# Kernel optimization log

Measured on AMD Instinct MI355X. Metric: run time of the kernel, lower is better.

## Reference

```python
import jax, jax.numpy as jnp
import numpy as np

B, S, CTX, DIM, NH, FFN, NE, TOPK = 2, 2048, 512, 1536, 12, 6144, 4, 2
HD = DIM // NH
EPS = 1e-6


def lin(x, w, b):
    return jnp.einsum('...d,od->...o', x, w) + b


def rmsnorm(x, w):
    xf = x.astype(jnp.float32)
    n = xf * jax.lax.rsqrt(jnp.mean(xf * xf, axis=-1, keepdims=True) + EPS)
    return n.astype(x.dtype) * w


def layernorm(x, w=None, b=None):
    m = jnp.mean(x, -1, keepdims=True)
    v = jnp.mean((x - m) ** 2, -1, keepdims=True)
    y = (x - m) * jax.lax.rsqrt(v + EPS)
    return y if w is None else y * w + b


def rope(x, cos, sin):
    # x: [B,S,DIM]; complex rotation on consecutive pairs per head
    b, s, _ = x.shape
    xr = x.reshape(b, s, NH, HD // 2, 2)
    xa, xb = xr[..., 0], xr[..., 1]
    c = cos[None, :, None, :]
    sn = sin[None, :, None, :]
    return jnp.stack([xa * c - xb * sn, xa * sn + xb * c], -1).reshape(b, s, DIM)


def sdpa(q, k, v):
    # scaled dot-product attention, q:[B,Sq,DIM], k/v:[B,Sk,DIM]
    b, sq, D = q.shape
    sk = k.shape[1]
    qh = q.reshape(b, sq, NH, HD).transpose(0, 2, 1, 3)
    kh = k.reshape(b, sk, NH, HD).transpose(0, 2, 1, 3)
    vh = v.reshape(b, sk, NH, HD).transpose(0, 2, 1, 3)
    scores = jnp.einsum('bnqd,bnkd->bnqk', qh, kh) * np.float32(1.0 / np.sqrt(HD))
    o = jnp.einsum('bnqk,bnkd->bnqd', jax.nn.softmax(scores, -1), vh)
    return o.transpose(0, 2, 1, 3).reshape(b, sq, D)


def _forward(x, context, t_mod, freqs_cos, freqs_sin, expert_weights,
             sa_q_w, sa_q_b, sa_k_w, sa_k_b, sa_v_w, sa_v_b, sa_o_w, sa_o_b, sa_nq_w, sa_nk_w,
             ca_q_w, ca_q_b, ca_k_w, ca_k_b, ca_v_w, ca_v_b, ca_o_w, ca_o_b, ca_nq_w, ca_nk_w,
             norm3_w, norm3_b, ffn_w1, ffn_b1, ffn_w2, ffn_b2, modulation, moe_w, moe_b,
             top_k_indices):
    mod = modulation + t_mod  # [B,6,DIM]
    shift_msa, scale_msa, gate_msa, shift_mlp, scale_mlp, gate_mlp = jnp.split(mod, 6, axis=1)
    # self-attention with AdaLN modulation + RoPE
    h = layernorm(x) * (1 + scale_msa) + shift_msa
    q = rope(rmsnorm(lin(h, sa_q_w, sa_q_b), sa_nq_w), freqs_cos, freqs_sin)
    k = rope(rmsnorm(lin(h, sa_k_w, sa_k_b), sa_nk_w), freqs_cos, freqs_sin)
    v = lin(h, sa_v_w, sa_v_b)
    x = x + gate_msa * lin(sdpa(q, k, v), sa_o_w, sa_o_b)
    # cross-attention (norm3 has affine params)
    h3 = layernorm(x, norm3_w, norm3_b)
    cq = rmsnorm(lin(h3, ca_q_w, ca_q_b), ca_nq_w)
    ck = rmsnorm(lin(context, ca_k_w, ca_k_b), ca_nk_w)
    cv = lin(context, ca_v_w, ca_v_b)
    x = x + lin(sdpa(cq, ck, cv), ca_o_w, ca_o_b)
    # FFN + MoE branch on the modulated input
    h2 = layernorm(x) * (1 + scale_mlp) + shift_mlp
    ff = lin(jax.nn.gelu(lin(h2, ffn_w1, ffn_b1), approximate=True), ffn_w2, ffn_b2)
    # MoE: compute ALL experts densely (as original), then gather-combine top-k
    eo = jnp.einsum('bsd,eod->bseo', h2, moe_w) + moe_b[None, None]  # [B,S,E,DIM]
    sel = jnp.take_along_axis(eo, top_k_indices[..., None], axis=2)  # [B,S,K,DIM]
    moe_out = jnp.sum(expert_weights[..., None] * sel, axis=2)
    x = x + gate_mlp * (ff + moe_out)
    return x


def setup_inputs() -> dict:
    key = jax.random.key(0)
    ks = iter(jax.random.split(key, 64))
    def rn(shape, scale=0.02):
        return jax.random.normal(next(ks), shape, dtype=jnp.float32) * scale
    pos = jnp.arange(S, dtype=jnp.float32)
    inv = 1.0 / (10000.0 ** (jnp.arange(0, HD, 2, dtype=jnp.float32) / HD))
    ang = pos[:, None] * inv[None, :]  # [S, HD//2]
    ew = jax.random.uniform(next(ks), (B, S, TOPK), dtype=jnp.float32) + 0.1
    ew = ew / jnp.sum(ew, -1, keepdims=True)
    inp = {
        'x': rn((B, S, DIM), 1.0),
        'context': rn((B, CTX, DIM), 1.0),
        't_mod': rn((B, 6, DIM), 1.0),
        'freqs_cos': jnp.cos(ang),
        'freqs_sin': jnp.sin(ang),
        'expert_weights': ew,
        'top_k_indices': jax.random.randint(next(ks), (B, S, TOPK), 0, NE, dtype=jnp.int32),
        'sa_q_w': rn((DIM, DIM)), 'sa_q_b': jnp.zeros((DIM,), jnp.float32),
        'sa_k_w': rn((DIM, DIM)), 'sa_k_b': jnp.zeros((DIM,), jnp.float32),
        'sa_v_w': rn((DIM, DIM)), 'sa_v_b': jnp.zeros((DIM,), jnp.float32),
        'sa_o_w': rn((DIM, DIM)), 'sa_o_b': jnp.zeros((DIM,), jnp.float32),
        'sa_nq_w': jnp.ones((DIM,), jnp.float32), 'sa_nk_w': jnp.ones((DIM,), jnp.float32),
        'ca_q_w': rn((DIM, DIM)), 'ca_q_b': jnp.zeros((DIM,), jnp.float32),
        'ca_k_w': rn((DIM, DIM)), 'ca_k_b': jnp.zeros((DIM,), jnp.float32),
        'ca_v_w': rn((DIM, DIM)), 'ca_v_b': jnp.zeros((DIM,), jnp.float32),
        'ca_o_w': rn((DIM, DIM)), 'ca_o_b': jnp.zeros((DIM,), jnp.float32),
        'ca_nq_w': jnp.ones((DIM,), jnp.float32), 'ca_nk_w': jnp.ones((DIM,), jnp.float32),
        'norm3_w': jnp.ones((DIM,), jnp.float32), 'norm3_b': jnp.zeros((DIM,), jnp.float32),
        'ffn_w1': rn((FFN, DIM)), 'ffn_b1': jnp.zeros((FFN,), jnp.float32),
        'ffn_w2': rn((DIM, FFN)), 'ffn_b2': jnp.zeros((DIM,), jnp.float32),
        'modulation': rn((1, 6, DIM), 1.0 / np.sqrt(DIM)),
        'moe_w': rn((NE, DIM, DIM)), 'moe_b': jnp.zeros((NE, DIM), jnp.float32),
    }
    return inp


def reference(x, context, t_mod, freqs_cos, freqs_sin, expert_weights, top_k_indices,
              sa_q_w, sa_q_b, sa_k_w, sa_k_b, sa_v_w, sa_v_b, sa_o_w, sa_o_b, sa_nq_w, sa_nk_w,
              ca_q_w, ca_q_b, ca_k_w, ca_k_b, ca_v_w, ca_v_b, ca_o_w, ca_o_b, ca_nq_w, ca_nk_w,
              norm3_w, norm3_b, ffn_w1, ffn_b1, ffn_w2, ffn_b2, modulation, moe_w, moe_b):
    return _forward(x, context, t_mod, freqs_cos, freqs_sin, expert_weights,
                    sa_q_w, sa_q_b, sa_k_w, sa_k_b, sa_v_w, sa_v_b, sa_o_w, sa_o_b, sa_nq_w, sa_nk_w,
                    ca_q_w, ca_q_b, ca_k_w, ca_k_b, ca_v_w, ca_v_b, ca_o_w, ca_o_b, ca_nq_w, ca_nk_w,
                    norm3_w, norm3_b, ffn_w1, ffn_b1, ffn_w2, ffn_b2, modulation, moe_w, moe_b,
                    top_k_indices)
```

## Files before the change

kernel.cpp:

```cpp
#include <hip/hip_runtime.h>
#include <cstdint>
#include <cstddef>

#define B_SZ 2
#define S_LEN 2048
#define CTX_LEN 512
#define DIM 1536
#define NH 12
#define HD 128
#define FFN_D 6144
#define NE 4
#define TOPK 2

typedef unsigned short u16;
typedef __attribute__((ext_vector_type(8))) __bf16 bf16x8;
typedef __attribute__((ext_vector_type(4))) float f32x4;
typedef __attribute__((ext_vector_type(4))) unsigned short u16x4;

__device__ __forceinline__ u16 f2bf(float f) {
  union { float f; uint32_t u; } un; un.f = f;
  uint32_t u = un.u;
  u += 0x7fffu + ((u >> 16) & 1u);
  return (u16)(u >> 16);
}

__global__ void cvt_f32_bf16(const float* __restrict__ src, u16* __restrict__ dst, int n4) {
  int i = blockIdx.x * blockDim.x + threadIdx.x;
  int stride = gridDim.x * blockDim.x;
  for (; i < n4; i += stride) {
    f32x4 v = ((const f32x4*)src)[i];
    u16x4 o;
    o.x = f2bf(v.x); o.y = f2bf(v.y); o.z = f2bf(v.z); o.w = f2bf(v.w);
    ((u16x4*)dst)[i] = o;
  }
}

template<int MODE>
__global__ __launch_bounds__(256) void ln_mod_kernel(
    const float* __restrict__ x, u16* __restrict__ out,
    const float* __restrict__ modv, const float* __restrict__ tmod,
    int scale_idx, int shift_idx,
    const float* __restrict__ w, const float* __restrict__ bvec)
{
  __shared__ float rbuf[8];
  int row = blockIdx.x;
  int b = row / S_LEN;
  const float* xr = x + (size_t)row * DIM;
  float v[6];
  float s = 0.f, s2 = 0.f;
#pragma unroll
  for (int j = 0; j < 6; ++j) {
    float t = xr[threadIdx.x + j * 256];
    v[j] = t; s += t; s2 += t * t;
  }
#pragma unroll
  for (int m = 32; m > 0; m >>= 1) { s += __shfl_xor(s, m, 64); s2 += __shfl_xor(s2, m, 64); }
  int wid = threadIdx.x >> 6;
  if ((threadIdx.x & 63) == 0) { rbuf[wid] = s; rbuf[4 + wid] = s2; }
  __syncthreads();
  s  = rbuf[0] + rbuf[1] + rbuf[2] + rbuf[3];
  s2 = rbuf[4] + rbuf[5] + rbuf[6] + rbuf[7];
  float mean = s * (1.f / DIM);
  float var  = s2 * (1.f / DIM) - mean * mean;
  float rstd = rsqrtf(var + 1e-6f);
#pragma unroll
  for (int j = 0; j < 6; ++j) {
    int n = threadIdx.x + j * 256;
    float y = (v[j] - mean) * rstd;
    float mul, add;
    if (MODE == 0) {
      mul = 1.f + modv[scale_idx * DIM + n] + tmod[(b * 6 + scale_idx) * DIM + n];
      add = modv[shift_idx * DIM + n] + tmod[(b * 6 + shift_idx) * DIM + n];
    } else {
      mul = w[n]; add = bvec[n];
    }
    out[(size_t)row * DIM + n] = f2bf(y * mul + add);
  }
}

template<int ROPE>
__global__ __launch_bounds__(256) void rms_rope_kernel(
    const float* __restrict__ x, const float* __restrict__ w,
    const float* __restrict__ cosb, const float* __restrict__ sinb,
    u16* __restrict__ out)
{
  __shared__ float rbuf[4];
  int row = blockIdx.x;
  const float* xr = x + (size_t)row * DIM;
  float v[6];
  float s2 = 0.f;
#pragma unroll
  for (int j = 0; j < 6; ++j) { float t = xr[threadIdx.x + j * 256]; v[j] = t; s2 += t * t; }
#pragma unroll
  for (int m = 32; m > 0; m >>= 1) s2 += __shfl_xor(s2, m, 64);
  int wid = threadIdx.x >> 6;
  if ((threadIdx.x & 63) == 0) rbuf[wid] = s2;
  __syncthreads();
  s2 = rbuf[0] + rbuf[1] + rbuf[2] + rbuf[3];
  float rs = rsqrtf(s2 * (1.f / DIM) + 1e-6f);
  if (ROPE) {
    int spos = row & (S_LEN - 1);
#pragma unroll
    for (int j = 0; j < 3; ++j) {
      int pr = threadIdx.x + j * 256;
      int head = pr >> 6, d = pr & 63;
      int n0 = head * HD + 2 * d;
      float xa = xr[n0] * rs * w[n0];
      float xb = xr[n0 + 1] * rs * w[n0 + 1];
      float c = cosb[spos * 64 + d], sn = sinb[spos * 64 + d];
      out[(size_t)row * DIM + n0]     = f2bf(xa * c - xb * sn);
      out[(size_t)row * DIM + n0 + 1] = f2bf(xa * sn + xb * c);
    }
  } else {
#pragma unroll
    for (int j = 0; j < 6; ++j) {
      int n = threadIdx.x + j * 256;
      out[(size_t)row * DIM + n] = f2bf(v[j] * rs * w[n]);
    }
  }
}

#define BKP 40

template<int EPI>
__global__ __launch_bounds__(256) void gemm_bt(
    const u16* __restrict__ A, const u16* __restrict__ W,
    const float* __restrict__ bias, void* __restrict__ Cout,
    const float* __restrict__ res,
    const float* __restrict__ modv, const float* __restrict__ tmod, int mod_idx,
    const float* __restrict__ ew, const int* __restrict__ topk, int expert,
    int M, int N, int K)
{
  __shared__ __align__(16) u16 As[128 * BKP];
  __shared__ __align__(16) u16 Bs[128 * BKP];
  int tid = threadIdx.x;
  int wid = tid >> 6, lane = tid & 63;
  int wr = wid >> 1, wc = wid & 1;
  size_t brow = (size_t)blockIdx.x * 128, bcol = (size_t)blockIdx.y * 128;

  f32x4 acc[4][4];
#pragma unroll
  for (int i = 0; i < 4; ++i)
#pragma unroll
    for (int j = 0; j < 4; ++j) acc[i][j] = (f32x4){0.f, 0.f, 0.f, 0.f};

  int flat0 = (wid * 64 + lane) * 8;
  int flat1 = flat0 + 2048;
  int r0 = flat0 >> 5, c0 = flat0 & 31;
  int r1 = flat1 >> 5, c1 = flat1 & 31;
  const u16* Ab0 = A + (brow + r0) * (size_t)K + c0;
  const u16* Ab1 = A + (brow + r1) * (size_t)K + c1;
  const u16* Wb0 = W + (bcol + r0) * (size_t)K + c0;
  const u16* Wb1 = W + (bcol + r1) * (size_t)K + c1;

  int cl = lane & 15, kk = (lane >> 4) * 8;

  for (int k0 = 0; k0 < K; k0 += 32) {
    bf16x8 a0 = *(const bf16x8*)(Ab0 + k0);
    bf16x8 a1 = *(const bf16x8*)(Ab1 + k0);
    bf16x8 b0 = *(const bf16x8*)(Wb0 + k0);
    bf16x8 b1 = *(const bf16x8*)(Wb1 + k0);
    __syncthreads();
    *(bf16x8*)&As[r0 * BKP + c0] = a0;
    *(bf16x8*)&As[r1 * BKP + c1] = a1;
    *(bf16x8*)&Bs[r0 * BKP + c0] = b0;
    *(bf16x8*)&Bs[r1 * BKP + c1] = b1;
    __syncthreads();
    bf16x8 af[4], bw[4];
#pragma unroll
    for (int i = 0; i < 4; ++i) {
      af[i] = *(const bf16x8*)&As[(wr * 64 + i * 16 + cl) * BKP + kk];
      bw[i] = *(const bf16x8*)&Bs[(wc * 64 + i * 16 + cl) * BKP + kk];
    }
#pragma unroll
    for (int mi = 0; mi < 4; ++mi)
#pragma unroll
      for (int ni = 0; ni < 4; ++ni)
        acc[mi][ni] = __builtin_amdgcn_mfma_f32_16x16x32_bf16(af[mi], bw[ni], acc[mi][ni], 0, 0, 0);
  }

  size_t row_base = brow + wr * 64;
  size_t col_base = bcol + wc * 64;
  int g4 = (lane >> 4) * 4;
#pragma unroll
  for (int ni = 0; ni < 4; ++ni) {
    size_t col = col_base + ni * 16 + cl;
    float bv = bias[col];
#pragma unroll
    for (int mi = 0; mi < 4; ++mi) {
#pragma unroll
      for (int r = 0; r < 4; ++r) {
        size_t row = row_base + mi * 16 + g4 + r;
        float val = acc[mi][ni][r] + bv;
        size_t idx = row * (size_t)N + col;
        if (EPI == 0) {
          ((float*)Cout)[idx] = val;
        } else if (EPI == 1) {
          ((u16*)Cout)[idx] = f2bf(val);
        } else if (EPI == 2) {
          float g = 0.5f * val * (1.f + tanhf(0.7978845608028654f * (val + 0.044715f * val * val * val)));
          ((u16*)Cout)[idx] = f2bf(g);
        } else if (EPI == 3) {
          int bb = (int)(row / S_LEN);
          float gate = modv[mod_idx * DIM + col] + tmod[((size_t)bb * 6 + mod_idx) * DIM + col];
          ((float*)Cout)[idx] = res[idx] + gate * val;
        } else if (EPI == 4) {
          ((float*)Cout)[idx] = res[idx] + val;
        } else if (EPI == 5) {
          float wsum = 0.f;
          int t0 = topk[row * TOPK], t1 = topk[row * TOPK + 1];
          if (t0 == expert) wsum += ew[row * TOPK];
          if (t1 == expert) wsum += ew[row * TOPK + 1];
          if (wsum != 0.f) ((float*)Cout)[idx] += wsum * val;
        }
      }
    }
  }
}

__global__ void transpose_v_kernel(const u16* __restrict__ v, u16* __restrict__ vt, int slen) {
  __shared__ u16 t[32][33];
  int bh = blockIdx.z;
  int b = bh / NH, h = bh % NH;
  int s0 = blockIdx.x * 32, d0 = blockIdx.y * 32;
  t[threadIdx.y][threadIdx.x] =
      v[((size_t)(b * slen) + s0 + threadIdx.y) * DIM + h * HD + d0 + threadIdx.x];
  __syncthreads();
  vt[((size_t)bh * HD + d0 + threadIdx.y) * slen + s0 + threadIdx.x] = t[threadIdx.x][threadIdx.y];
}

__global__ __launch_bounds__(256) void flash_attn_kernel(
    const u16* __restrict__ q, const u16* __restrict__ k,
    const u16* __restrict__ vt, u16* __restrict__ out,
    int sq, int sk)
{
  __shared__ __align__(16) u16 p_lds[4][16][32];
  int tid = threadIdx.x;
  int wid = tid >> 6, lane = tid & 63;
  int cl = lane & 15, g = lane >> 4;
  int bh = blockIdx.y, b = bh / NH, h = bh % NH;
  int q0 = blockIdx.x * 64 + wid * 16;

  const u16* qp = q + ((size_t)(b * sq) + q0 + cl) * DIM + h * HD + g * 8;
  bf16x8 aq[4];
#pragma unroll
  for (int c = 0; c < 4; ++c) aq[c] = *(const bf16x8*)(qp + c * 32);

  f32x4 o[8];
#pragma unroll
  for (int i = 0; i < 8; ++i) o[i] = (f32x4){0.f, 0.f, 0.f, 0.f};
  float m_r[4] = {-1e30f, -1e30f, -1e30f, -1e30f};
  float l_r[4] = {0.f, 0.f, 0.f, 0.f};
  const float sc = 0.08838834764831845f;

  const u16* kb = k + (size_t)(b * sk) * DIM + h * HD;
  const u16* vb = vt + (size_t)bh * HD * sk;

  for (int kt = 0; kt < sk; kt += 32) {
    f32x4 s0v = (f32x4){0.f, 0.f, 0.f, 0.f};
    f32x4 s1v = (f32x4){0.f, 0.f, 0.f, 0.f};
    const u16* kp0 = kb + (size_t)(kt + cl) * DIM + g * 8;
    const u16* kp1 = kp0 + (size_t)16 * DIM;
#pragma unroll
    for (int c = 0; c < 4; ++c) {
      bf16x8 bk0 = *(const bf16x8*)(kp0 + c * 32);
      bf16x8 bk1 = *(const bf16x8*)(kp1 + c * 32);
      s0v = __builtin_amdgcn_mfma_f32_16x16x32_bf16(aq[c], bk0, s0v, 0, 0, 0);
      s1v = __builtin_amdgcn_mfma_f32_16x16x32_bf16(aq[c], bk1, s1v, 0, 0, 0);
    }
    float p0[4], p1[4];
#pragma unroll
    for (int r = 0; r < 4; ++r) {
      float v0 = s0v[r] * sc, v1 = s1v[r] * sc;
      float pm = fmaxf(v0, v1);
#pragma unroll
      for (int msk = 8; msk > 0; msk >>= 1) pm = fmaxf(pm, __shfl_xor(pm, msk, 64));
      float mn = fmaxf(m_r[r], pm);
      float cf = __expf(m_r[r] - mn);
      float e0 = __expf(v0 - mn), e1 = __expf(v1 - mn);
      float rsum = e0 + e1;
#pragma unroll
      for (int msk = 8; msk > 0; msk >>= 1) rsum += __shfl_xor(rsum, msk, 64);
      l_r[r] = l_r[r] * cf + rsum;
      m_r[r] = mn;
      p0[r] = e0; p1[r] = e1;
#pragma unroll
      for (int cc = 0; cc < 8; ++cc) o[cc][r] *= cf;
    }
#pragma unroll
    for (int r = 0; r < 4; ++r) {
      p_lds[wid][g * 4 + r][cl]      = f2bf(p0[r]);
      p_lds[wid][g * 4 + r][16 + cl] = f2bf(p1[r]);
    }
    asm volatile("s_waitcnt lgkmcnt(0)" ::: "memory");
    bf16x8 ap = *(const bf16x8*)&p_lds[wid][cl][g * 8];
    const u16* vp = vb + (size_t)cl * sk + kt + g * 8;
#pragma unroll
    for (int cc = 0; cc < 8; ++cc) {
      bf16x8 bv = *(const bf16x8*)(vp + (size_t)cc * 16 * sk);
      o[cc] = __builtin_amdgcn_mfma_f32_16x16x32_bf16(ap, bv, o[cc], 0, 0, 0);
    }
  }
#pragma unroll
  for (int r = 0; r < 4; ++r) {
    float inv = 1.f / l_r[r];
    size_t orow = (size_t)(b * sq) + q0 + g * 4 + r;
#pragma unroll
    for (int cc = 0; cc < 8; ++cc)
      out[orow * DIM + h * HD + cc * 16 + cl] = f2bf(o[cc][r] * inv);
  }
}

__global__ __launch_bounds__(256) void final_add_kernel(
    const float* __restrict__ xb, float* __restrict__ out,
    const float* __restrict__ modv, const float* __restrict__ tmod)
{
  size_t i4 = (size_t)blockIdx.x * 256 + threadIdx.x;
  size_t base = i4 * 4;
  int n = (int)(base % DIM);
  int b = (int)(base / ((size_t)S_LEN * DIM));
  f32x4 xv = ((const f32x4*)xb)[i4];
  f32x4 ov = ((const f32x4*)out)[i4];
  f32x4 r;
#pragma unroll
  for (int j = 0; j < 4; ++j) {
    float gate = modv[5 * DIM + n + j] + tmod[((size_t)b * 6 + 5) * DIM + n + j];
    r[j] = xv[j] + gate * ov[j];
  }
  ((f32x4*)out)[i4] = r;
}

extern "C" void kernel_launch(void* const* d_in, const int* in_sizes, int n_in,
                              void* d_out, int out_size, void* d_ws, size_t ws_size,
                              hipStream_t stream) {
  (void)in_sizes; (void)n_in; (void)out_size; (void)ws_size;
  const float* x_in   = (const float*)d_in[0];
  const float* ctx_in = (const float*)d_in[1];
  const float* tmod   = (const float*)d_in[2];
  const float* fcos   = (const float*)d_in[3];
  const float* fsin   = (const float*)d_in[4];
  const float* ew     = (const float*)d_in[5];
  const int*   topk   = (const int*)d_in[6];
  const float* sa_q_w = (const float*)d_in[7];
  const float* sa_q_b = (const float*)d_in[8];
  const float* sa_k_w = (const float*)d_in[9];
  const float* sa_k_b = (const float*)d_in[10];
  const float* sa_v_w = (const float*)d_in[11];
  const float* sa_v_b = (const float*)d_in[12];
  const float* sa_o_w = (const float*)d_in[13];
  const float* sa_o_b = (const float*)d_in[14];
  const float* sa_nq_w = (const float*)d_in[15];
  const float* sa_nk_w = (const float*)d_in[16];
  const float* ca_q_w = (const float*)d_in[17];
  const float* ca_q_b = (const float*)d_in[18];
  const float* ca_k_w = (const float*)d_in[19];
  const float* ca_k_b = (const float*)d_in[20];
  const float* ca_v_w = (const float*)d_in[21];
  const float* ca_v_b = (const float*)d_in[22];
  const float* ca_o_w = (const float*)d_in[23];
  const float* ca_o_b = (const float*)d_in[24];
  const float* ca_nq_w = (const float*)d_in[25];
  const float* ca_nk_w = (const float*)d_in[26];
  const float* norm3_w = (const float*)d_in[27];
  const float* norm3_b = (const float*)d_in[28];
  const float* ffn_w1 = (const float*)d_in[29];
  const float* ffn_b1 = (const float*)d_in[30];
  const float* ffn_w2 = (const float*)d_in[31];
  const float* ffn_b2 = (const float*)d_in[32];
  const float* modv   = (const float*)d_in[33];
  const float* moe_w  = (const float*)d_in[34];
  const float* moe_b  = (const float*)d_in[35];

  char* p = (char*)d_ws;
  auto alloc = [&](size_t bytes) { void* r = (void*)p; p += ((bytes + 255) & ~(size_t)255); return r; };
  const size_t NTOK = (size_t)B_SZ * S_LEN;
  const size_t NCTX = (size_t)B_SZ * CTX_LEN;
  const size_t DD = (size_t)DIM * DIM;

  u16* w_saq  = (u16*)alloc(DD * 2);
  u16* w_sak  = (u16*)alloc(DD * 2);
  u16* w_sav  = (u16*)alloc(DD * 2);
  u16* w_sao  = (u16*)alloc(DD * 2);
  u16* w_caq  = (u16*)alloc(DD * 2);
  u16* w_cak  = (u16*)alloc(DD * 2);
  u16* w_cav  = (u16*)alloc(DD * 2);
  u16* w_cao  = (u16*)alloc(DD * 2);
  u16* w_ffn1 = (u16*)alloc((size_t)FFN_D * DIM * 2);
  u16* w_ffn2 = (u16*)alloc((size_t)DIM * FFN_D * 2);
  u16* w_moe  = (u16*)alloc((size_t)NE * DD * 2);
  u16* h_bf   = (u16*)alloc(NTOK * DIM * 2);
  float* raw  = (float*)alloc(NTOK * DIM * 4);
  float* xb   = (float*)alloc(NTOK * DIM * 4);
  u16* q_bf   = (u16*)alloc(NTOK * DIM * 2);
  u16* k_bf   = (u16*)alloc(NTOK * DIM * 2);
  u16* v_bf   = (u16*)alloc(NTOK * DIM * 2);
  u16* vt_bf  = (u16*)alloc(NTOK * DIM * 2);
  u16* ctx_bf = (u16*)alloc(NCTX * DIM * 2);
  u16* ck_bf  = (u16*)alloc(NCTX * DIM * 2);
  u16* cv_bf  = (u16*)alloc(NCTX * DIM * 2);
  u16* attn_bf = (u16*)raw;
  u16* ff1_bf  = q_bf;

  auto cvtl = [&](const float* s_, u16* d_, size_t n) {
    int n4 = (int)(n / 4);
    int nb = (n4 + 255) / 256; if (nb > 2048) nb = 2048;
    cvt_f32_bf16<<<nb, 256, 0, stream>>>(s_, d_, n4);
  };
  auto GEMM = [&](int epi, const u16* Aa, const u16* Ww, const float* bb, void* Cc,
                  const float* rr, int mod_idx, int expert, int M, int N, int K) {
    dim3 g(M / 128, N / 128);
    switch (epi) {
      case 0: gemm_bt<0><<<g, 256, 0, stream>>>(Aa, Ww, bb, Cc, rr, modv, tmod, mod_idx, ew, topk, expert, M, N, K); break;
      case 1: gemm_bt<1><<<g, 256, 0, stream>>>(Aa, Ww, bb, Cc, rr, modv, tmod, mod_idx, ew, topk, expert, M, N, K); break;
      case 2: gemm_bt<2><<<g, 256, 0, stream>>>(Aa, Ww, bb, Cc, rr, modv, tmod, mod_idx, ew, topk, expert, M, N, K); break;
      case 3: gemm_bt<3><<<g, 256, 0, stream>>>(Aa, Ww, bb, Cc, rr, modv, tmod, mod_idx, ew, topk, expert, M, N, K); break;
      case 4: gemm_bt<4><<<g, 256, 0, stream>>>(Aa, Ww, bb, Cc, rr, modv, tmod, mod_idx, ew, topk, expert, M, N, K); break;
      case 5: gemm_bt<5><<<g, 256, 0, stream>>>(Aa, Ww, bb, Cc, rr, modv, tmod, mod_idx, ew, topk, expert, M, N, K); break;
    }
  };

  cvtl(sa_q_w, w_saq, DD); cvtl(sa_k_w, w_sak, DD); cvtl(sa_v_w, w_sav, DD); cvtl(sa_o_w, w_sao, DD);
  cvtl(ca_q_w, w_caq, DD); cvtl(ca_k_w, w_cak, DD); cvtl(ca_v_w, w_cav, DD); cvtl(ca_o_w, w_cao, DD);
  cvtl(ffn_w1, w_ffn1, (size_t)FFN_D * DIM);
  cvtl(ffn_w2, w_ffn2, (size_t)DIM * FFN_D);
  cvtl(moe_w, w_moe, (size_t)NE * DD);
  cvtl(ctx_in, ctx_bf, NCTX * DIM);

  ln_mod_kernel<0><<<(int)NTOK, 256, 0, stream>>>(x_in, h_bf, modv, tmod, 1, 0, nullptr, nullptr);
  GEMM(0, h_bf, w_saq, sa_q_b, raw, nullptr, 0, 0, (int)NTOK, DIM, DIM);
  rms_rope_kernel<1><<<(int)NTOK, 256, 0, stream>>>(raw, sa_nq_w, fcos, fsin, q_bf);
  GEMM(0, h_bf, w_sak, sa_k_b, raw, nullptr, 0, 0, (int)NTOK, DIM, DIM);
  rms_rope_kernel<1><<<(int)NTOK, 256, 0, stream>>>(raw, sa_nk_w, fcos, fsin, k_bf);
  GEMM(1, h_bf, w_sav, sa_v_b, v_bf, nullptr, 0, 0, (int)NTOK, DIM, DIM);
  transpose_v_kernel<<<dim3(S_LEN / 32, HD / 32, B_SZ * NH), dim3(32, 32), 0, stream>>>(v_bf, vt_bf, S_LEN);
  flash_attn_kernel<<<dim3(S_LEN / 64, B_SZ * NH), 256, 0, stream>>>(q_bf, k_bf, vt_bf, attn_bf, S_LEN, S_LEN);
  GEMM(3, attn_bf, w_sao, sa_o_b, xb, x_in, 2, 0, (int)NTOK, DIM, DIM);

  ln_mod_kernel<1><<<(int)NTOK, 256, 0, stream>>>(xb, h_bf, nullptr, nullptr, 0, 0, norm3_w, norm3_b);
  GEMM(0, h_bf, w_caq, ca_q_b, raw, nullptr, 0, 0, (int)NTOK, DIM, DIM);
  rms_rope_kernel<0><<<(int)NTOK, 256, 0, stream>>>(raw, ca_nq_w, fcos, fsin, q_bf);
  GEMM(0, ctx_bf, w_cak, ca_k_b, raw, nullptr, 0, 0, (int)NCTX, DIM, DIM);
  rms_rope_kernel<0><<<(int)NCTX, 256, 0, stream>>>(raw, ca_nk_w, fcos, fsin, ck_bf);
  GEMM(1, ctx_bf, w_cav, ca_v_b, cv_bf, nullptr, 0, 0, (int)NCTX, DIM, DIM);
  transpose_v_kernel<<<dim3(CTX_LEN / 32, HD / 32, B_SZ * NH), dim3(32, 32), 0, stream>>>(cv_bf, vt_bf, CTX_LEN);
  flash_attn_kernel<<<dim3(S_LEN / 64, B_SZ * NH), 256, 0, stream>>>(q_bf, ck_bf, vt_bf, attn_bf, S_LEN, CTX_LEN);
  GEMM(4, attn_bf, w_cao, ca_o_b, xb, xb, 0, 0, (int)NTOK, DIM, DIM);

  ln_mod_kernel<0><<<(int)NTOK, 256, 0, stream>>>(xb, h_bf, modv, tmod, 4, 3, nullptr, nullptr);
  GEMM(2, h_bf, w_ffn1, ffn_b1, ff1_bf, nullptr, 0, 0, (int)NTOK, FFN_D, DIM);
  GEMM(0, ff1_bf, w_ffn2, ffn_b2, d_out, nullptr, 0, 0, (int)NTOK, DIM, FFN_D);
  for (int e = 0; e < NE; ++e)
    GEMM(5, h_bf, w_moe + (size_t)e * DD, moe_b + (size_t)e * DIM, d_out, nullptr, 0, e, (int)NTOK, DIM, DIM);
  final_add_kernel<<<(int)(NTOK * DIM / 4 / 256), 256, 0, stream>>>(xb, (float*)d_out, modv, tmod);
}
```

Before: 1.789 ms.

## Use direct global-to-LDS loads in GEMM and stage K tiles in flash attention

The GEMM now loads A and W tiles through global_load_lds, straight into unpadded LDS, instead of going through registers, and adds a trailing barrier. Flash attention now double-buffers 64-key K tiles in swizzled LDS using direct loads, processes 64 keys per step, and reads the doubled P through a padded LDS buffer. The softmax scale is folded into q during the RMS-norm kernels, and GELU-tanh is rewritten with exp and a fast reciprocal. Dropping the padding may bring LDS bank conflicts in the GEMM fragment reads, and the bf16 rounding of q changes slightly.

New measurement: 1.621 ms. 9.4% less time.

```diff
diff --git a/kernel.cpp b/kernel.cpp
--- a/kernel.cpp
+++ b/kernel.cpp
@@ -22,6 +22,12 @@
   uint32_t u = un.u;
   u += 0x7fffu + ((u >> 16) & 1u);
   return (u16)(u >> 16);
+}
+
+__device__ __forceinline__ void gload_lds16(const u16* g, u16* l) {
+  __builtin_amdgcn_global_load_lds(
+      (const __attribute__((address_space(1))) void*)g,
+      (__attribute__((address_space(3))) void*)l, 16, 0, 0);
 }
 
 __global__ void cvt_f32_bf16(const float* __restrict__ src, u16* __restrict__ dst, int n4) {
@@ -78,7 +84,8 @@
   }
 }
 
-template<int ROPE>
+#define ATT_SC 0.08838834764831845f
+template<int ROPE, int SCQ>
 __global__ __launch_bounds__(256) void rms_rope_kernel(
     const float* __restrict__ x, const float* __restrict__ w,
     const float* __restrict__ cosb, const float* __restrict__ sinb,
@@ -98,6 +105,7 @@
   __syncthreads();
   s2 = rbuf[0] + rbuf[1] + rbuf[2] + rbuf[3];
   float rs = rsqrtf(s2 * (1.f / DIM) + 1e-6f);
+  const float osc = SCQ ? ATT_SC : 1.f;
   if (ROPE) {
     int spos = row & (S_LEN - 1);
 #pragma unroll
@@ -108,19 +116,17 @@
       float xa = xr[n0] * rs * w[n0];
       float xb = xr[n0 + 1] * rs * w[n0 + 1];
       float c = cosb[spos * 64 + d], sn = sinb[spos * 64 + d];
-      out[(size_t)row * DIM + n0]     = f2bf(xa * c - xb * sn);
-      out[(size_t)row * DIM + n0 + 1] = f2bf(xa * sn + xb * c);
+      out[(size_t)row * DIM + n0]     = f2bf((xa * c - xb * sn) * osc);
+      out[(size_t)row * DIM + n0 + 1] = f2bf((xa * sn + xb * c) * osc);
     }
   } else {
 #pragma unroll
     for (int j = 0; j < 6; ++j) {
       int n = threadIdx.x + j * 256;
-      out[(size_t)row * DIM + n] = f2bf(v[j] * rs * w[n]);
-    }
-  }
-}
-
-#define BKP 40
+      out[(size_t)row * DIM + n] = f2bf(v[j] * rs * w[n] * osc);
+    }
+  }
+}
 
 template<int EPI>
 __global__ __launch_bounds__(256) void gemm_bt(
@@ -131,8 +137,8 @@
     const float* __restrict__ ew, const int* __restrict__ topk, int expert,
     int M, int N, int K)
 {
-  __shared__ __align__(16) u16 As[128 * BKP];
-  __shared__ __align__(16) u16 Bs[128 * BKP];
+  __shared__ __align__(16) u16 As[128 * 32];
+  __shared__ __align__(16) u16 Bs[128 * 32];
   int tid = threadIdx.x;
   int wid = tid >> 6, lane = tid & 63;
   int wr = wid >> 1, wc = wid & 1;
@@ -144,39 +150,33 @@
 #pragma unroll
     for (int j = 0; j < 4; ++j) acc[i][j] = (f32x4){0.f, 0.f, 0.f, 0.f};
 
-  int flat0 = (wid * 64 + lane) * 8;
-  int flat1 = flat0 + 2048;
-  int r0 = flat0 >> 5, c0 = flat0 & 31;
-  int r1 = flat1 >> 5, c1 = flat1 & 31;
-  const u16* Ab0 = A + (brow + r0) * (size_t)K + c0;
-  const u16* Ab1 = A + (brow + r1) * (size_t)K + c1;
-  const u16* Wb0 = W + (bcol + r0) * (size_t)K + c0;
-  const u16* Wb1 = W + (bcol + r1) * (size_t)K + c1;
+  int srow = wid * 16 + (lane >> 2);
+  int scol = (lane & 3) * 8;
+  const u16* Ag0 = A + (brow + srow) * (size_t)K + scol;
+  const u16* Wg0 = W + (bcol + srow) * (size_t)K + scol;
+  u16* Al0 = &As[wid * 512];
+  u16* Bl0 = &Bs[wid * 512];
 
   int cl = lane & 15, kk = (lane >> 4) * 8;
 
   for (int k0 = 0; k0 < K; k0 += 32) {
-    bf16x8 a0 = *(const bf16x8*)(Ab0 + k0);
-    bf16x8 a1 = *(const bf16x8*)(Ab1 + k0);
-    bf16x8 b0 = *(const bf16x8*)(Wb0 + k0);
-    bf16x8 b1 = *(const bf16x8*)(Wb1 + k0);
-    __syncthreads();
-    *(bf16x8*)&As[r0 * BKP + c0] = a0;
-    *(bf16x8*)&As[r1 * BKP + c1] = a1;
-    *(bf16x8*)&Bs[r0 * BKP + c0] = b0;
-    *(bf16x8*)&Bs[r1 * BKP + c1] = b1;
+    gload_lds16(Ag0 + k0, Al0);
+    gload_lds16(Ag0 + (size_t)64 * K + k0, Al0 + 2048);
+    gload_lds16(Wg0 + k0, Bl0);
+    gload_lds16(Wg0 + (size_t)64 * K + k0, Bl0 + 2048);
     __syncthreads();
     bf16x8 af[4], bw[4];
 #pragma unroll
     for (int i = 0; i < 4; ++i) {
-      af[i] = *(const bf16x8*)&As[(wr * 64 + i * 16 + cl) * BKP + kk];
-      bw[i] = *(const bf16x8*)&Bs[(wc * 64 + i * 16 + cl) * BKP + kk];
+      af[i] = *(const bf16x8*)&As[(wr * 64 + i * 16 + cl) * 32 + kk];
+      bw[i] = *(const bf16x8*)&Bs[(wc * 64 + i * 16 + cl) * 32 + kk];
     }
 #pragma unroll
     for (int mi = 0; mi < 4; ++mi)
 #pragma unroll
       for (int ni = 0; ni < 4; ++ni)
         acc[mi][ni] = __builtin_amdgcn_mfma_f32_16x16x32_bf16(af[mi], bw[ni], acc[mi][ni], 0, 0, 0);
+    __syncthreads();
   }
 
   size_t row_base = brow + wr * 64;
@@ -198,7 +198,8 @@
         } else if (EPI == 1) {
           ((u16*)Cout)[idx] = f2bf(val);
         } else if (EPI == 2) {
-          float g = 0.5f * val * (1.f + tanhf(0.7978845608028654f * (val + 0.044715f * val * val * val)));
+          float u = 0.7978845608028654f * (val + 0.044715f * val * val * val);
+          float g = val * __builtin_amdgcn_rcpf(1.f + __expf(-2.f * u));
           ((u16*)Cout)[idx] = f2bf(g);
         } else if (EPI == 3) {
           int bb = (int)(row / S_LEN);
@@ -234,7 +235,8 @@
     const u16* __restrict__ vt, u16* __restrict__ out,
     int sq, int sk)
 {
-  __shared__ __align__(16) u16 p_lds[4][16][32];
+  __shared__ __align__(16) u16 Ks[2][64 * 128];
+  __shared__ __align__(16) u16 p_lds[4][16 * 72];
   int tid = threadIdx.x;
   int wid = tid >> 6, lane = tid & 63;
   int cl = lane & 15, g = lane >> 4;
@@ -251,55 +253,76 @@
   for (int i = 0; i < 8; ++i) o[i] = (f32x4){0.f, 0.f, 0.f, 0.f};
   float m_r[4] = {-1e30f, -1e30f, -1e30f, -1e30f};
   float l_r[4] = {0.f, 0.f, 0.f, 0.f};
-  const float sc = 0.08838834764831845f;
 
   const u16* kb = k + (size_t)(b * sk) * DIM + h * HD;
   const u16* vb = vt + (size_t)bh * HD * sk;
 
-  for (int kt = 0; kt < sk; kt += 32) {
-    f32x4 s0v = (f32x4){0.f, 0.f, 0.f, 0.f};
-    f32x4 s1v = (f32x4){0.f, 0.f, 0.f, 0.f};
-    const u16* kp0 = kb + (size_t)(kt + cl) * DIM + g * 8;
-    const u16* kp1 = kp0 + (size_t)16 * DIM;
-#pragma unroll
-    for (int c = 0; c < 4; ++c) {
-      bf16x8 bk0 = *(const bf16x8*)(kp0 + c * 32);
-      bf16x8 bk1 = *(const bf16x8*)(kp1 + c * 32);
-      s0v = __builtin_amdgcn_mfma_f32_16x16x32_bf16(aq[c], bk0, s0v, 0, 0, 0);
-      s1v = __builtin_amdgcn_mfma_f32_16x16x32_bf16(aq[c], bk1, s1v, 0, 0, 0);
-    }
-    float p0[4], p1[4];
+  int u_sw = (lane & 15) ^ ((4 * (wid & 1) + (lane >> 4)) & 7);
+  const u16* ksrc0 = kb + (size_t)(4 * wid + (lane >> 4)) * DIM + u_sw * 8;
+
+  int nt = sk / 64;
+  int x8 = (cl & 7) * 8;
+  int buf = 0;
+
+#pragma unroll
+  for (int i = 0; i < 4; ++i)
+    gload_lds16(ksrc0 + (size_t)(16 * i) * DIM, &Ks[0][(i * 4 + wid) * 512]);
+
+  for (int t = 0; t < nt; ++t) {
+    __syncthreads();
+    if (t + 1 < nt) {
+      const u16* s0 = ksrc0 + (size_t)(t + 1) * 64 * DIM;
+#pragma unroll
+      for (int i = 0; i < 4; ++i)
+        gload_lds16(s0 + (size_t)(16 * i) * DIM, &Ks[buf ^ 1][(i * 4 + wid) * 512]);
+    }
+    const u16* Kt = Ks[buf];
+    f32x4 s[4];
+#pragma unroll
+    for (int ct = 0; ct < 4; ++ct) {
+      s[ct] = (f32x4){0.f, 0.f, 0.f, 0.f};
+      int keyb = (ct * 16 + cl) * 128;
+#pragma unroll
+      for (int c = 0; c < 4; ++c) {
+        bf16x8 kf = *(const bf16x8*)&Kt[keyb + ((c * 32 + g * 8) ^ x8)];
+        s[ct] = __builtin_amdgcn_mfma_f32_16x16x32_bf16(aq[c], kf, s[ct], 0, 0, 0);
+      }
+    }
 #pragma unroll
     for (int r = 0; r < 4; ++r) {
-      float v0 = s0v[r] * sc, v1 = s1v[r] * sc;
-      float pm = fmaxf(v0, v1);
+      float v0 = s[0][r], v1 = s[1][r], v2 = s[2][r], v3 = s[3][r];
+      float pm = fmaxf(fmaxf(v0, v1), fmaxf(v2, v3));
 #pragma unroll
       for (int msk = 8; msk > 0; msk >>= 1) pm = fmaxf(pm, __shfl_xor(pm, msk, 64));
       float mn = fmaxf(m_r[r], pm);
       float cf = __expf(m_r[r] - mn);
       float e0 = __expf(v0 - mn), e1 = __expf(v1 - mn);
-      float rsum = e0 + e1;
+      float e2 = __expf(v2 - mn), e3 = __expf(v3 - mn);
+      float rsum = (e0 + e1) + (e2 + e3);
 #pragma unroll
       for (int msk = 8; msk > 0; msk >>= 1) rsum += __shfl_xor(rsum, msk, 64);
       l_r[r] = l_r[r] * cf + rsum;
       m_r[r] = mn;
-      p0[r] = e0; p1[r] = e1;
 #pragma unroll
       for (int cc = 0; cc < 8; ++cc) o[cc][r] *= cf;
-    }
-#pragma unroll
-    for (int r = 0; r < 4; ++r) {
-      p_lds[wid][g * 4 + r][cl]      = f2bf(p0[r]);
-      p_lds[wid][g * 4 + r][16 + cl] = f2bf(p1[r]);
+      int pr = (g * 4 + r) * 72;
+      p_lds[wid][pr + cl]      = f2bf(e0);
+      p_lds[wid][pr + 16 + cl] = f2bf(e1);
+      p_lds[wid][pr + 32 + cl] = f2bf(e2);
+      p_lds[wid][pr + 48 + cl] = f2bf(e3);
     }
     asm volatile("s_waitcnt lgkmcnt(0)" ::: "memory");
-    bf16x8 ap = *(const bf16x8*)&p_lds[wid][cl][g * 8];
-    const u16* vp = vb + (size_t)cl * sk + kt + g * 8;
+    bf16x8 ap0 = *(const bf16x8*)&p_lds[wid][cl * 72 + g * 8];
+    bf16x8 ap1 = *(const bf16x8*)&p_lds[wid][cl * 72 + 32 + g * 8];
+    const u16* vp = vb + (size_t)cl * sk + t * 64 + g * 8;
 #pragma unroll
     for (int cc = 0; cc < 8; ++cc) {
-      bf16x8 bv = *(const bf16x8*)(vp + (size_t)cc * 16 * sk);
-      o[cc] = __builtin_amdgcn_mfma_f32_16x16x32_bf16(ap, bv, o[cc], 0, 0, 0);
-    }
+      bf16x8 bv0 = *(const bf16x8*)(vp + (size_t)cc * 16 * sk);
+      bf16x8 bv1 = *(const bf16x8*)(vp + (size_t)cc * 16 * sk + 32);
+      o[cc] = __builtin_amdgcn_mfma_f32_16x16x32_bf16(ap0, bv0, o[cc], 0, 0, 0);
+      o[cc] = __builtin_amdgcn_mfma_f32_16x16x32_bf16(ap1, bv1, o[cc], 0, 0, 0);
+    }
+    buf ^= 1;
   }
 #pragma unroll
   for (int r = 0; r < 4; ++r) {
@@ -428,9 +451,9 @@
 
   ln_mod_kernel<0><<<(int)NTOK, 256, 0, stream>>>(x_in, h_bf, modv, tmod, 1, 0, nullptr, nullptr);
   GEMM(0, h_bf, w_saq, sa_q_b, raw, nullptr, 0, 0, (int)NTOK, DIM, DIM);
-  rms_rope_kernel<1><<<(int)NTOK, 256, 0, stream>>>(raw, sa_nq_w, fcos, fsin, q_bf);
+  rms_rope_kernel<1, 1><<<(int)NTOK, 256, 0, stream>>>(raw, sa_nq_w, fcos, fsin, q_bf);
   GEMM(0, h_bf, w_sak, sa_k_b, raw, nullptr, 0, 0, (int)NTOK, DIM, DIM);
-  rms_rope_kernel<1><<<(int)NTOK, 256, 0, stream>>>(raw, sa_nk_w, fcos, fsin, k_bf);
+  rms_rope_kernel<1, 0><<<(int)NTOK, 256, 0, stream>>>(raw, sa_nk_w, fcos, fsin, k_bf);
   GEMM(1, h_bf, w_sav, sa_v_b, v_bf, nullptr, 0, 0, (int)NTOK, DIM, DIM);
   transpose_v_kernel<<<dim3(S_LEN / 32, HD / 32, B_SZ * NH), dim3(32, 32), 0, stream>>>(v_bf, vt_bf, S_LEN);
   flash_attn_kernel<<<dim3(S_LEN / 64, B_SZ * NH), 256, 0, stream>>>(q_bf, k_bf, vt_bf, attn_bf, S_LEN, S_LEN);
@@ -438,9 +461,9 @@
 
   ln_mod_kernel<1><<<(int)NTOK, 256, 0, stream>>>(xb, h_bf, nullptr, nullptr, 0, 0, norm3_w, norm3_b);
   GEMM(0, h_bf, w_caq, ca_q_b, raw, nullptr, 0, 0, (int)NTOK, DIM, DIM);
-  rms_rope_kernel<0><<<(int)NTOK, 256, 0, stream>>>(raw, ca_nq_w, fcos, fsin, q_bf);
+  rms_rope_kernel<0, 1><<<(int)NTOK, 256, 0, stream>>>(raw, ca_nq_w, fcos, fsin, q_bf);
   GEMM(0, ctx_bf, w_cak, ca_k_b, raw, nullptr, 0, 0, (int)NCTX, DIM, DIM);
-  rms_rope_kernel<0><<<(int)NCTX, 256, 0, stream>>>(raw, ca_nk_w, fcos, fsin, ck_bf);
+  rms_rope_kernel<0, 0><<<(int)NCTX, 256, 0, stream>>>(raw, ca_nk_w, fcos, fsin, ck_bf);
   GEMM(1, ctx_bf, w_cav, ca_v_b, cv_bf, nullptr, 0, 0, (int)NCTX, DIM, DIM);
   transpose_v_kernel<<<dim3(CTX_LEN / 32, HD / 32, B_SZ * NH), dim3(32, 32), 0, stream>>>(cv_bf, vt_bf, CTX_LEN);
   flash_attn_kernel<<<dim3(S_LEN / 64, B_SZ * NH), 256, 0, stream>>>(q_bf, ck_bf, vt_bf, attn_bf, S_LEN, CTX_LEN);
```
